# Kernel optimization log

Hardware: AMD Instinct MI355X
Metric: run time of the kernel (lower is better)

## Reference

```python
import jax, jax.numpy as jnp
import numpy as np

DIM = 768
HEADS = 12


def setup_inputs() -> dict:
    key = jax.random.key(0)
    ks = jax.random.split(key, 7)
    bs, nmm, nv, na = 32, 256, 196, 60
    s = DIM ** -0.5
    return {
        "xmm": jax.random.normal(ks[0], (bs, nmm, DIM), jnp.float32),
        "xv": jax.random.normal(ks[1], (bs, nv, DIM), jnp.float32),
        "xa": jax.random.normal(ks[2], (bs, na, DIM), jnp.float32),
        "Wq": jax.random.normal(ks[3], (DIM, DIM), jnp.float32) * s,
        "Wkv": jax.random.normal(ks[4], (DIM, 2 * DIM), jnp.float32) * s,
        "Wproj": jax.random.normal(ks[5], (DIM, DIM), jnp.float32) * s,
        "bproj": jnp.zeros((DIM,), jnp.float32),
    }


def reference(xmm, xv, xa, Wq, Wkv, Wproj, bproj):
    bs, nmm, dim = xmm.shape
    hd = dim // HEADS
    scale = hd ** -0.5
    x_src = jnp.concatenate([xv, xa], axis=1)            # [bs, nv+na, dim]
    q = (xmm @ Wq).reshape(bs, nmm, HEADS, hd).transpose(0, 2, 1, 3)   # [b,h,q,d]
    kv = (x_src @ Wkv).reshape(bs, -1, 2, HEADS, hd).transpose(2, 0, 3, 1, 4)
    k, v = kv[0], kv[1]                                  # [b,h,k,d]
    attn = jax.nn.softmax(jnp.einsum('bhqd,bhkd->bhqk', q, k) * scale, axis=-1)
    out = jnp.einsum('bhqk,bhkd->bhqd', attn, v)
    out = out.transpose(0, 2, 1, 3).reshape(bs, nmm, dim)
    out = out @ Wproj + bproj
    return out, attn
```

## Files before the change

### kernel.cpp

```cpp
#include <hip/hip_runtime.h>


typedef __attribute__((ext_vector_type(8))) _Float16 f16x8;
typedef __attribute__((ext_vector_type(4))) _Float16 f16x4;
typedef __attribute__((ext_vector_type(4))) float    f32x4;

#define AS1 __attribute__((address_space(1)))
#define AS3 __attribute__((address_space(3)))

__device__ __forceinline__ void gload_lds16(const void* g, void* l) {
    void* gnc = const_cast<void*>(g);
    __builtin_amdgcn_global_load_lds((AS1 void*)gnc, (AS3 void*)l, 16, 0, 0);
}

__global__ __launch_bounds__(256) void prep_acts(const float* __restrict__ xmm,
                                                 const float* __restrict__ xv,
                                                 const float* __restrict__ xa,
                                                 _Float16* __restrict__ xmm16,
                                                 _Float16* __restrict__ xsrc16) {
    int id = blockIdx.x * 256 + threadIdx.x;
    float4 v;
    _Float16* dst;
    int off;
    if (id < 1572864) {
        v = ((const float4*)xmm)[id];
        dst = xmm16; off = id;
    } else {
        int t = id - 1572864;
        int c4 = t % 192;
        int r  = (t / 192) & 255;
        int b  = t / 49152;
        if (r < 196) v = ((const float4*)xv)[((long)b * 196 + r) * 192 + c4];
        else         v = ((const float4*)xa)[((long)b * 60 + (r - 196)) * 192 + c4];
        dst = xsrc16; off = t;
    }
    f16x4 h = { (_Float16)v.x, (_Float16)v.y, (_Float16)v.z, (_Float16)v.w };
    ((f16x4*)dst)[off] = h;
}

__global__ __launch_bounds__(256) void prep_weights(const float* __restrict__ Wq,
                                                    const float* __restrict__ Wkv,
                                                    const float* __restrict__ Wproj,
                                                    _Float16* __restrict__ WqT,
                                                    _Float16* __restrict__ WkvT,
                                                    _Float16* __restrict__ WprojT) {
    int id = blockIdx.x * 256 + threadIdx.x;
    if (id < 589824) {
        int k = id % 768, n = id / 768;
        WqT[id] = (_Float16)(0.125f * Wq[(long)k * 768 + n]);
        return;
    }
    id -= 589824;
    if (id < 1179648) {
        int k = id % 768, n = id / 768;
        WkvT[id] = (_Float16)Wkv[(long)k * 1536 + n];
        return;
    }
    id -= 1179648;
    if (id < 589824) {
        int k = id % 768, n = id / 768;
        WprojT[id] = (_Float16)Wproj[(long)k * 768 + n];
    }
}

template <int OUT_F32>
__device__ __forceinline__ void gemm_body(const _Float16* __restrict__ A,
                                          const _Float16* __restrict__ Bt,
                                          void* __restrict__ C,
                                          const float* __restrict__ bias,
                                          long bm, long bn, int N, int K) {
    __shared__ _Float16 As[128 * 64];
    __shared__ _Float16 Bs[128 * 64];

    const int tid  = threadIdx.x;
    const int wave = tid >> 6, lane = tid & 63;
    const int lrow = lane & 15, quad = lane >> 4;
    const int wm = (wave >> 1) * 64, wn = (wave & 1) * 64;

    f32x4 acc[4][4];
    const f32x4 fz = {0.f, 0.f, 0.f, 0.f};
#pragma unroll
    for (int mt = 0; mt < 4; ++mt)
#pragma unroll
        for (int nt = 0; nt < 4; ++nt) acc[mt][nt] = fz;

    for (int k0 = 0; k0 < K; k0 += 64) {
#pragma unroll
        for (int it = 0; it < 4; ++it) {
            int seg = tid + it * 256;
            int rr = seg >> 3, pp = seg & 7;
            int cc = ((pp ^ (rr & 7)) << 3);
            gload_lds16(A  + (bm + rr) * (long)K + k0 + cc, As + seg * 8);
            gload_lds16(Bt + (bn + rr) * (long)K + k0 + cc, Bs + seg * 8);
        }
        __syncthreads();
#pragma unroll
        for (int ks = 0; ks < 2; ++ks) {
            f16x8 af[4], bf[4];
#pragma unroll
            for (int mt = 0; mt < 4; ++mt) {
                int r = wm + mt * 16 + lrow;
                af[mt] = *(const f16x8*)(As + r * 64 + (((ks * 4 + quad) ^ (r & 7)) << 3));
            }
#pragma unroll
            for (int nt = 0; nt < 4; ++nt) {
                int r = wn + nt * 16 + lrow;
                bf[nt] = *(const f16x8*)(Bs + r * 64 + (((ks * 4 + quad) ^ (r & 7)) << 3));
            }
#pragma unroll
            for (int mt = 0; mt < 4; ++mt)
#pragma unroll
                for (int nt = 0; nt < 4; ++nt)
                    acc[mt][nt] = __builtin_amdgcn_mfma_f32_16x16x32_f16(
                        bf[nt], af[mt], acc[mt][nt], 0, 0, 0);
        }
        __syncthreads();
    }

#pragma unroll
    for (int mt = 0; mt < 4; ++mt) {
        long row = bm + wm + mt * 16 + lrow;
#pragma unroll
        for (int nt = 0; nt < 4; ++nt) {
            long col0 = bn + wn + nt * 16 + quad * 4;
            if (OUT_F32) {
                float4 b4 = *(const float4*)(bias + col0);
                float4 o = { acc[mt][nt][0] + b4.x, acc[mt][nt][1] + b4.y,
                             acc[mt][nt][2] + b4.z, acc[mt][nt][3] + b4.w };
                *(float4*)((float*)C + row * N + col0) = o;
            } else {
                f16x4 h = { (_Float16)acc[mt][nt][0], (_Float16)acc[mt][nt][1],
                            (_Float16)acc[mt][nt][2], (_Float16)acc[mt][nt][3] };
                *(f16x4*)((_Float16*)C + row * N + col0) = h;
            }
        }
    }
}

__global__ __launch_bounds__(256, 2)
void gemm_qkv(const _Float16* __restrict__ xmm16, const _Float16* __restrict__ xsrc16,
              const _Float16* __restrict__ WqT, const _Float16* __restrict__ WkvT,
              _Float16* __restrict__ Q16, _Float16* __restrict__ KV16) {
    const int bx = blockIdx.x;
    const long bm = (long)blockIdx.y * 128;
    if (bx < 6) gemm_body<0>(xmm16,  WqT,  (void*)Q16,  nullptr, bm, (long)bx * 128,       768,  768);
    else        gemm_body<0>(xsrc16, WkvT, (void*)KV16, nullptr, bm, (long)(bx - 6) * 128, 1536, 768);
}

__global__ __launch_bounds__(256, 2)
void gemm_proj(const _Float16* __restrict__ O16, const _Float16* __restrict__ WprojT,
               float* __restrict__ out, const float* __restrict__ bias) {
    gemm_body<1>(O16, WprojT, (void*)out, bias, (long)blockIdx.y * 128, (long)blockIdx.x * 128, 768, 768);
}

__global__ __launch_bounds__(256, 2)
void attn_kernel(const _Float16* __restrict__ Qg, const _Float16* __restrict__ KVg,
                 float* __restrict__ attn_out, _Float16* __restrict__ Og) {
    __shared__ _Float16 sh[32768];
    _Float16* Ks = sh;
    _Float16* Vt = sh + 16384;
    _Float16* Ps = sh;

    const int tid  = threadIdx.x;
    const int wave = tid >> 6, lane = tid & 63;
    const int lrow = lane & 15, quad = lane >> 4;
    const int qb = blockIdx.x, h = blockIdx.y, b = blockIdx.z;
    const long qrow0 = (long)b * 256 + qb * 64;
    const long krow0 = (long)b * 256;

    f16x8 aq[2];
#pragma unroll
    for (int ks = 0; ks < 2; ++ks)
        aq[ks] = *(const f16x8*)(Qg + (qrow0 + wave * 16 + lrow) * 768 + h * 64 + ks * 32 + quad * 8);

#pragma unroll
    for (int it = 0; it < 8; ++it) {
        int seg = tid + it * 256;
        int rr = seg >> 3, pp = seg & 7;
        int cc = ((pp ^ (rr & 7)) << 3);
        gload_lds16(KVg + (krow0 + rr) * 1536 + h * 64 + cc, Ks + seg * 8);
    }
#pragma unroll
    for (int it = 0; it < 8; ++it) {
        int seg = tid + it * 256;
        int key = seg >> 3, d0 = (seg & 7) * 8;
        f16x8 v = *(const f16x8*)(KVg + (krow0 + key) * 1536 + 768 + h * 64 + d0);
#pragma unroll
        for (int i = 0; i < 8; ++i) {
            int d = d0 + i;
            Vt[d * 256 + ((((key >> 3) ^ (d & 7)) << 3) | (key & 7))] = v[i];
        }
    }
    __syncthreads();

    f32x4 sacc[16];
    const f32x4 fz = {0.f, 0.f, 0.f, 0.f};
#pragma unroll
    for (int nt = 0; nt < 16; ++nt) sacc[nt] = fz;
#pragma unroll
    for (int ks = 0; ks < 2; ++ks) {
#pragma unroll
        for (int nt = 0; nt < 16; ++nt) {
            int r = nt * 16 + lrow;
            f16x8 bk = *(const f16x8*)(Ks + r * 64 + (((ks * 4 + quad) ^ (r & 7)) << 3));
            sacc[nt] = __builtin_amdgcn_mfma_f32_16x16x32_f16(bk, aq[ks], sacc[nt], 0, 0, 0);
        }
    }

    float m = -1e30f;
#pragma unroll
    for (int nt = 0; nt < 16; ++nt)
#pragma unroll
        for (int j = 0; j < 4; ++j) m = fmaxf(m, sacc[nt][j]);
    m = fmaxf(m, __shfl_xor(m, 16));
    m = fmaxf(m, __shfl_xor(m, 32));
    float s = 0.f;
#pragma unroll
    for (int nt = 0; nt < 16; ++nt)
#pragma unroll
        for (int j = 0; j < 4; ++j) {
            float p = __expf(sacc[nt][j] - m);
            sacc[nt][j] = p; s += p;
        }
    s += __shfl_xor(s, 16);
    s += __shfl_xor(s, 32);
    const float li = 1.f / s;

    __syncthreads();

    const long abase = (((long)b * 12 + h) * 256 + qb * 64) * 256;
    const int q = wave * 16 + lrow;
#pragma unroll
    for (int nt = 0; nt < 16; ++nt) {
        float4 o = { sacc[nt][0] * li, sacc[nt][1] * li, sacc[nt][2] * li, sacc[nt][3] * li };
        *(float4*)(attn_out + abase + (long)q * 256 + nt * 16 + quad * 4) = o;
        f16x4 hp = { (_Float16)o.x, (_Float16)o.y, (_Float16)o.z, (_Float16)o.w };
        int blk = nt * 2 + (quad >> 1);
        *(f16x4*)(Ps + q * 256 + ((blk ^ (q & 7)) << 3) + ((quad & 1) << 2)) = hp;
    }
    __syncthreads();

    f32x4 oacc[4];
#pragma unroll
    for (int nt = 0; nt < 4; ++nt) oacc[nt] = fz;
#pragma unroll
    for (int ks = 0; ks < 8; ++ks) {
        int pr = wave * 16 + lrow;
        f16x8 ap = *(const f16x8*)(Ps + pr * 256 + (((ks * 4 + quad) ^ (pr & 7)) << 3));
#pragma unroll
        for (int nt = 0; nt < 4; ++nt) {
            int d = nt * 16 + lrow;
            f16x8 bv = *(const f16x8*)(Vt + d * 256 + (((ks * 4 + quad) ^ (d & 7)) << 3));
            oacc[nt] = __builtin_amdgcn_mfma_f32_16x16x32_f16(bv, ap, oacc[nt], 0, 0, 0);
        }
    }
#pragma unroll
    for (int nt = 0; nt < 4; ++nt) {
        f16x4 ho = { (_Float16)oacc[nt][0], (_Float16)oacc[nt][1],
                     (_Float16)oacc[nt][2], (_Float16)oacc[nt][3] };
        *(f16x4*)(Og + (qrow0 + wave * 16 + lrow) * 768 + h * 64 + nt * 16 + quad * 4) = ho;
    }
}

extern "C" void kernel_launch(void* const* d_in, const int* in_sizes, int n_in,
                              void* d_out, int out_size, void* d_ws, size_t ws_size,
                              hipStream_t stream) {
    const float* xmm   = (const float*)d_in[0];
    const float* xv    = (const float*)d_in[1];
    const float* xa    = (const float*)d_in[2];
    const float* Wq    = (const float*)d_in[3];
    const float* Wkv   = (const float*)d_in[4];
    const float* Wproj = (const float*)d_in[5];
    const float* bproj = (const float*)d_in[6];

    float* out  = (float*)d_out;
    float* attn = out + 6291456;

    char* ws = (char*)d_ws;
    _Float16* xmm16  = (_Float16*)(ws);
    _Float16* xsrc16 = (_Float16*)(ws + 12582912);
    _Float16* WqT    = (_Float16*)(ws + 25165824);
    _Float16* WkvT   = (_Float16*)(ws + 26345472);
    _Float16* WprojT = (_Float16*)(ws + 28704768);
    _Float16* Q16    = (_Float16*)(ws + 29884416);
    _Float16* KV16   = (_Float16*)(ws + 42467328);
    _Float16* O16    = xmm16;

    prep_acts   <<<12288, 256, 0, stream>>>(xmm, xv, xa, xmm16, xsrc16);
    prep_weights<<<9216,  256, 0, stream>>>(Wq, Wkv, Wproj, WqT, WkvT, WprojT);

    gemm_qkv<<<dim3(18, 64), 256, 0, stream>>>(xmm16, xsrc16, WqT, WkvT, Q16, KV16);

    attn_kernel<<<dim3(4, 12, 32), 256, 0, stream>>>(Q16, KV16, attn, O16);

    gemm_proj<<<dim3(6, 64), 256, 0, stream>>>(O16, WprojT, out, bproj);
}
```

Baseline: 293.8 us.

## Fuse prep kernels with tiled weight transpose, remap block order for XCD locality

Merges the activation and weight conversion kernels into one launch. The weight transpose now goes through a 64x64 LDS tile, so both the global reads and the writes are coalesced instead of strided. The GEMM and attention kernels switch to a 1D grid with a remap that groups consecutive logical tiles onto the same XCD (block index mod 8), aiming to improve L2 reuse of shared weight and KV tiles. One attention __syncthreads is replaced by an explicit lgkmcnt wait plus s_barrier.

```diff
diff --git a/kernel.cpp b/kernel.cpp
--- a/kernel.cpp
+++ b/kernel.cpp
@@ -13,53 +13,62 @@
     __builtin_amdgcn_global_load_lds((AS1 void*)gnc, (AS3 void*)l, 16, 0, 0);
 }
 
-__global__ __launch_bounds__(256) void prep_acts(const float* __restrict__ xmm,
-                                                 const float* __restrict__ xv,
-                                                 const float* __restrict__ xa,
-                                                 _Float16* __restrict__ xmm16,
-                                                 _Float16* __restrict__ xsrc16) {
-    int id = blockIdx.x * 256 + threadIdx.x;
-    float4 v;
-    _Float16* dst;
-    int off;
-    if (id < 1572864) {
-        v = ((const float4*)xmm)[id];
-        dst = xmm16; off = id;
-    } else {
-        int t = id - 1572864;
-        int c4 = t % 192;
-        int r  = (t / 192) & 255;
-        int b  = t / 49152;
-        if (r < 196) v = ((const float4*)xv)[((long)b * 196 + r) * 192 + c4];
-        else         v = ((const float4*)xa)[((long)b * 60 + (r - 196)) * 192 + c4];
-        dst = xsrc16; off = t;
-    }
-    f16x4 h = { (_Float16)v.x, (_Float16)v.y, (_Float16)v.z, (_Float16)v.w };
-    ((f16x4*)dst)[off] = h;
-}
-
-__global__ __launch_bounds__(256) void prep_weights(const float* __restrict__ Wq,
-                                                    const float* __restrict__ Wkv,
-                                                    const float* __restrict__ Wproj,
-                                                    _Float16* __restrict__ WqT,
-                                                    _Float16* __restrict__ WkvT,
-                                                    _Float16* __restrict__ WprojT) {
-    int id = blockIdx.x * 256 + threadIdx.x;
-    if (id < 589824) {
-        int k = id % 768, n = id / 768;
-        WqT[id] = (_Float16)(0.125f * Wq[(long)k * 768 + n]);
+__global__ __launch_bounds__(256) void prep_all(const float* __restrict__ xmm,
+                                                const float* __restrict__ xv,
+                                                const float* __restrict__ xa,
+                                                const float* __restrict__ Wq,
+                                                const float* __restrict__ Wkv,
+                                                const float* __restrict__ Wproj,
+                                                _Float16* __restrict__ xmm16,
+                                                _Float16* __restrict__ xsrc16,
+                                                _Float16* __restrict__ WqT,
+                                                _Float16* __restrict__ WkvT,
+                                                _Float16* __restrict__ WprojT) {
+    __shared__ _Float16 wlds[64][72];
+    int bid = blockIdx.x;
+    if (bid < 12288) {
+        int id = bid * 256 + threadIdx.x;
+        float4 v;
+        _Float16* dst;
+        int off;
+        if (id < 1572864) {
+            v = ((const float4*)xmm)[id];
+            dst = xmm16; off = id;
+        } else {
+            int t = id - 1572864;
+            int c4 = t % 192;
+            int r  = (t / 192) & 255;
+            int b  = t / 49152;
+            if (r < 196) v = ((const float4*)xv)[((long)b * 196 + r) * 192 + c4];
+            else         v = ((const float4*)xa)[((long)b * 60 + (r - 196)) * 192 + c4];
+            dst = xsrc16; off = t;
+        }
+        f16x4 h = { (_Float16)v.x, (_Float16)v.y, (_Float16)v.z, (_Float16)v.w };
+        ((f16x4*)dst)[off] = h;
         return;
     }
-    id -= 589824;
-    if (id < 1179648) {
-        int k = id % 768, n = id / 768;
-        WkvT[id] = (_Float16)Wkv[(long)k * 1536 + n];
-        return;
-    }
-    id -= 1179648;
-    if (id < 589824) {
-        int k = id % 768, n = id / 768;
-        WprojT[id] = (_Float16)Wproj[(long)k * 768 + n];
+    int t = bid - 12288;
+    const float* src; _Float16* dst; int W; float scale; int tk, tn;
+    if (t < 144)      { src = Wq;    dst = WqT;    W = 768;  scale = 0.125f; tk = t % 12;  tn = t / 12; }
+    else if (t < 432) { int u = t - 144; src = Wkv;   dst = WkvT;   W = 1536; scale = 1.0f; tk = u % 12; tn = u / 12; }
+    else              { int u = t - 432; src = Wproj; dst = WprojT; W = 768;  scale = 1.0f; tk = u % 12; tn = u / 12; }
+    const int tk0 = tk * 64, tn0 = tn * 64;
+    const int rloc = threadIdx.x >> 4, c0 = (threadIdx.x & 15) * 4;
+#pragma unroll
+    for (int i = 0; i < 4; ++i) {
+        int k = tk0 + rloc + 16 * i;
+        float4 v = *(const float4*)(src + (long)k * W + tn0 + c0);
+        wlds[c0 + 0][rloc + 16 * i] = (_Float16)(v.x * scale);
+        wlds[c0 + 1][rloc + 16 * i] = (_Float16)(v.y * scale);
+        wlds[c0 + 2][rloc + 16 * i] = (_Float16)(v.z * scale);
+        wlds[c0 + 3][rloc + 16 * i] = (_Float16)(v.w * scale);
+    }
+    __syncthreads();
+#pragma unroll
+    for (int i = 0; i < 4; ++i) {
+        int nloc = rloc + 16 * i;
+        f16x4 h = *(const f16x4*)(&wlds[nloc][c0]);
+        *(f16x4*)(dst + (long)(tn0 + nloc) * 768 + tk0 + c0) = h;
     }
 }
 
@@ -141,8 +150,10 @@
 void gemm_qkv(const _Float16* __restrict__ xmm16, const _Float16* __restrict__ xsrc16,
               const _Float16* __restrict__ WqT, const _Float16* __restrict__ WkvT,
               _Float16* __restrict__ Q16, _Float16* __restrict__ KV16) {
-    const int bx = blockIdx.x;
-    const long bm = (long)blockIdx.y * 128;
+    const int f = blockIdx.x;
+    const int w = ((f & 7) * 144) + (f >> 3);
+    const int bx = w % 18;
+    const long bm = (long)(w / 18) * 128;
     if (bx < 6) gemm_body<0>(xmm16,  WqT,  (void*)Q16,  nullptr, bm, (long)bx * 128,       768,  768);
     else        gemm_body<0>(xsrc16, WkvT, (void*)KV16, nullptr, bm, (long)(bx - 6) * 128, 1536, 768);
 }
@@ -150,7 +161,11 @@
 __global__ __launch_bounds__(256, 2)
 void gemm_proj(const _Float16* __restrict__ O16, const _Float16* __restrict__ WprojT,
                float* __restrict__ out, const float* __restrict__ bias) {
-    gemm_body<1>(O16, WprojT, (void*)out, bias, (long)blockIdx.y * 128, (long)blockIdx.x * 128, 768, 768);
+    const int f = blockIdx.x;
+    const int w = ((f & 7) * 48) + (f >> 3);
+    const int bx = w % 6;
+    const long bm = (long)(w / 6) * 128;
+    gemm_body<1>(O16, WprojT, (void*)out, bias, bm, (long)bx * 128, 768, 768);
 }
 
 __global__ __launch_bounds__(256, 2)
@@ -164,7 +179,11 @@
     const int tid  = threadIdx.x;
     const int wave = tid >> 6, lane = tid & 63;
     const int lrow = lane & 15, quad = lane >> 4;
-    const int qb = blockIdx.x, h = blockIdx.y, b = blockIdx.z;
+    const int f = blockIdx.x;
+    const int w = ((f & 7) * 192) + (f >> 3);
+    const int qb = w & 3;
+    const int hb = w >> 2;
+    const int h = hb % 12, b = hb / 12;
     const long qrow0 = (long)b * 256 + qb * 64;
     const long krow0 = (long)b * 256;
 
@@ -238,7 +257,9 @@
         int blk = nt * 2 + (quad >> 1);
         *(f16x4*)(Ps + q * 256 + ((blk ^ (q & 7)) << 3) + ((quad & 1) << 2)) = hp;
     }
-    __syncthreads();
+    asm volatile("s_waitcnt lgkmcnt(0)" ::: "memory");
+    __builtin_amdgcn_sched_barrier(0);
+    __builtin_amdgcn_s_barrier();
 
     f32x4 oacc[4];
 #pragma unroll
@@ -286,12 +307,12 @@
     _Float16* KV16   = (_Float16*)(ws + 42467328);
     _Float16* O16    = xmm16;
 
-    prep_acts   <<<12288, 256, 0, stream>>>(xmm, xv, xa, xmm16, xsrc16);
-    prep_weights<<<9216,  256, 0, stream>>>(Wq, Wkv, Wproj, WqT, WkvT, WprojT);
-
-    gemm_qkv<<<dim3(18, 64), 256, 0, stream>>>(xmm16, xsrc16, WqT, WkvT, Q16, KV16);
-
-    attn_kernel<<<dim3(4, 12, 32), 256, 0, stream>>>(Q16, KV16, attn, O16);
-
-    gemm_proj<<<dim3(6, 64), 256, 0, stream>>>(O16, WprojT, out, bproj);
-}
+    prep_all<<<12864, 256, 0, stream>>>(xmm, xv, xa, Wq, Wkv, Wproj,
+                                        xmm16, xsrc16, WqT, WkvT, WprojT);
+
+    gemm_qkv<<<1152, 256, 0, stream>>>(xmm16, xsrc16, WqT, WkvT, Q16, KV16);
+
+    attn_kernel<<<1536, 256, 0, stream>>>(Q16, KV16, attn, O16);
+
+    gemm_proj<<<384, 256, 0, stream>>>(O16, WprojT, out, bproj);
+}
```

Result: faster. 271.3 us (-7.7%).
